# Optimization experiments

Hardware: AMD Instinct MI355X
Metric: run time of the kernel (lower is better)

## Reference

```python
import jax, jax.numpy as jnp
import numpy as np

B, L, H, K = 16, 2048, 1024, 4  # batch, seq, hidden, heads
NEG = -1e9  # stand-in for -inf in masked softmax (grad-safe, prob ~0)

def setup_inputs() -> dict:
    key = jax.random.key(0)
    ks = jax.random.split(key, 6)
    s = 0.02
    hidden = jax.random.normal(ks[0], (B, L, H), dtype=jnp.float32)
    masks = jax.random.randint(ks[1], (B, L), 0, 2).astype(jnp.bool_)
    Wp = jax.random.normal(ks[2], (H, H * K), dtype=jnp.float32) * s
    W1 = jax.random.normal(ks[3], (K, H, H // 2), dtype=jnp.float32) * s
    b1 = jax.random.normal(ks[4], (K, H // 2), dtype=jnp.float32) * s
    W2 = jax.random.normal(ks[5], (K, H // 2), dtype=jnp.float32) * s
    return {"hidden": hidden, "masks": masks, "Wp": Wp, "W1": W1, "b1": b1, "W2": W2}

def reference(hidden, masks, Wp, W1, b1, W2):
    b, l, h = hidden.shape
    k = W1.shape[0]
    # projection (no bias), split into heads: [b,l,k,h]
    proj = (hidden @ Wp).reshape(b, l, k, h)
    # per-head tanh MLP score: Linear(h, h//2)+bias -> tanh -> Linear(h//2, 1)
    a1 = jnp.tanh(jnp.einsum('blkh,khd->blkd', proj, W1) + b1)  # [b,l,k,h//2]
    logits = jnp.einsum('blkd,kd->kbl', a1, W2)                 # [k,b,l]
    # masked softmax over sequence dim
    logits = jnp.where(masks[None, :, :], NEG, logits)
    attn = jax.nn.softmax(logits, axis=-1)                      # [k,b,l]
    return attn
```

## Files before the change

### kernel.cpp

```cpp
#include <hip/hip_runtime.h>
#include <hip/hip_bf16.h>
#include <cstdint>
#include <cstddef>

#define HD   1024
#define NK   4
#define DD   512
#define LSEQ 2048
#define NB   16
#define MTOT (NB*LSEQ)
#define NF2  (NK*DD)

typedef __attribute__((ext_vector_type(4))) float f32x4;
typedef __attribute__((ext_vector_type(8))) short bf16x8;

#define GLOAD16(gp, lp) __builtin_amdgcn_global_load_lds( \
    (const __attribute__((address_space(1))) void*)(gp),  \
    (__attribute__((address_space(3))) void*)(lp), 16, 0, 0)

static __device__ __forceinline__ ushort f2bf(float f) {
  union { float f; unsigned u; } x; x.f = f;
  unsigned r = x.u + 0x7FFFu + ((x.u >> 16) & 1u);
  return (ushort)(r >> 16);
}

static __device__ __forceinline__ float fast_tanh(float x) {
  x = fminf(fmaxf(x, -15.f), 15.f);
  float t = __expf(2.0f * x);
  return (t - 1.0f) / (t + 1.0f);
}

__global__ void detect_mask_kernel(const unsigned char* __restrict__ m, int nbytes,
                                   int* __restrict__ flag) {
  int found = 0;
  for (int i = blockIdx.x * blockDim.x + threadIdx.x; i < nbytes;
       i += gridDim.x * blockDim.x)
    if ((i & 3) && m[i]) found = 1;
  if (__any(found) && (threadIdx.x & 63) == 0) atomicOr(flag, 1);
}

__global__ void cvt_f32_bf16_kernel(const float* __restrict__ src,
                                    ushort* __restrict__ dst, long n) {
  long stride = (long)gridDim.x * blockDim.x * 4;
  for (long i = ((long)blockIdx.x * blockDim.x + threadIdx.x) * 4; i < n; i += stride) {
    f32x4 v = *(const f32x4*)(src + i);
    ushort4 o; o.x = f2bf(v.x); o.y = f2bf(v.y); o.z = f2bf(v.z); o.w = f2bf(v.w);
    *(ushort4*)(dst + i) = o;
  }
}

__global__ void cvt_wp_heads_kernel(const float* __restrict__ Wp,
                                    ushort* __restrict__ WpH) {
  long i4 = ((long)blockIdx.x * blockDim.x + threadIdx.x) * 4;
  int h = (int)(i4 >> 20);
  int c = (int)((i4 >> 10) & 1023);
  int j = (int)(i4 & 1023);
  f32x4 v = *(const f32x4*)(Wp + (long)c * (NK * HD) + h * HD + j);
  ushort4 o; o.x = f2bf(v.x); o.y = f2bf(v.y); o.z = f2bf(v.z); o.w = f2bf(v.w);
  *(ushort4*)(WpH + i4) = o;
}

__global__ void transpose_cvt_kernel(const float* __restrict__ src,
                                     ushort* __restrict__ dst,
                                     int R, int C, long sBatch, long dBatch) {
  __shared__ float tile[32][33];
  const float* s = src + blockIdx.z * sBatch;
  ushort* d = dst + blockIdx.z * dBatch;
  int c0 = blockIdx.x * 32, r0 = blockIdx.y * 32;
  int tx = threadIdx.x, ty = threadIdx.y;
  #pragma unroll
  for (int i = 0; i < 32; i += 8)
    tile[ty + i][tx] = s[(long)(r0 + ty + i) * C + (c0 + tx)];
  __syncthreads();
  #pragma unroll
  for (int i = 0; i < 32; i += 8)
    d[(long)(c0 + ty + i) * R + (r0 + tx)] = f2bf(tile[tx][ty + i]);
}

template<int MODE>
__global__ __launch_bounds__(512, 2)
void gemm256_kernel(const ushort* __restrict__ A, int lda, long aZs,
                    const ushort* __restrict__ Bt, int ldb, long bZs, int Kdim,
                    ushort* __restrict__ Cout, int ldc, long cZs,
                    const float* __restrict__ b1, const float* __restrict__ W2,
                    float* __restrict__ logitsOut, int m0glob) {
  __shared__ __align__(16) char lds[131072];

  const int tid = threadIdx.x;
  const int w = tid >> 6, lane = tid & 63;
  const int z = blockIdx.z;

  int bid = blockIdx.x + gridDim.x * blockIdx.y;
  const int nwg = gridDim.x * gridDim.y;
  if ((nwg & 7) == 0) {
    const int q = nwg >> 3;
    bid = (bid & 7) * q + (bid >> 3);
  }
  const int nMB = gridDim.x;
  const int m0 = (bid % nMB) * 256;
  const int n0 = (bid / nMB) * 256;

  const ushort* Ag = A + z * aZs + (long)m0 * lda;
  const ushort* Bg = Bt + z * bZs + (long)n0 * ldb;

  const int wm = w >> 2, wn = w & 3;
  const int rsel = lane & 15;
  const int chunkC = ((lane >> 4) ^ ((rsel >> 1) & 3)) << 4;
  const int laneA = wm * 8192 + rsel * 64 + chunkC;
  const int laneB = 65536 + wn * 4096 + rsel * 64 + chunkC;

  const int stCg = ((lane & 3) ^ ((lane >> 3) & 3)) * 8;
  const int stR0 = (w * 2) * 16 + (lane >> 2);
  const int stDst0 = (w * 2) * 1024;

  #define STAGE(gbase, ld, regionByte, dsl, h)                                  \
    {                                                                           \
      _Pragma("unroll")                                                         \
      for (int j = 0; j < 2; ++j) {                                             \
        const ushort* gp = (gbase) + (long)(stR0 + j * 16) * (ld) +             \
                           ((h) << 5) + stCg;                                   \
        GLOAD16(gp, lds + (regionByte) + (dsl) * 16384 + stDst0 + j * 1024);    \
      }                                                                         \
    }

  f32x4 acc[8][4] = {};
  const int nph = Kdim >> 5;

  #pragma unroll
  for (int h = 0; h < 3; ++h) {
    STAGE(Ag, lda, 0,     h, h);
    STAGE(Bg, ldb, 65536, h, h);
  }
  asm volatile("s_waitcnt vmcnt(4)" ::: "memory");
  __builtin_amdgcn_sched_barrier(0);
  __builtin_amdgcn_s_barrier();

  bf16x8 aCur[8], bCur[4], aNxt[8], bNxt[4];
  #pragma unroll
  for (int nf = 0; nf < 4; ++nf) bCur[nf] = *(const bf16x8*)(lds + laneB + nf * 1024);
  #pragma unroll
  for (int f = 0; f < 8; ++f)    aCur[f] = *(const bf16x8*)(lds + laneA + f * 1024);

  #define PHASE(g, CA, CB, NA, NB_)                                             \
    {                                                                           \
      const int dsl = ((g) + 3) & 3;                                            \
      const int hh = ((g) + 3 < nph) ? (g) + 3 : nph - 1;                       \
      STAGE(Ag, lda, 0,     dsl, hh);                                           \
      STAGE(Bg, ldb, 65536, dsl, hh);                                           \
      const int rs = (((g) + 1) & 3) << 14;                                     \
      _Pragma("unroll")                                                         \
      for (int nf = 0; nf < 4; ++nf)                                            \
        NB_[nf] = *(const bf16x8*)(lds + rs + laneB + nf * 1024);               \
      _Pragma("unroll")                                                         \
      for (int f = 0; f < 8; ++f)                                               \
        NA[f] = *(const bf16x8*)(lds + rs + laneA + f * 1024);                  \
      asm volatile("s_waitcnt lgkmcnt(12)" ::: "memory");                       \
      __builtin_amdgcn_sched_barrier(0);                                        \
      __builtin_amdgcn_s_setprio(1);                                            \
      _Pragma("unroll")                                                         \
      for (int f = 0; f < 8; ++f)                                               \
        _Pragma("unroll")                                                       \
        for (int nf = 0; nf < 4; ++nf)                                          \
          acc[f][nf] = __builtin_amdgcn_mfma_f32_16x16x32_bf16(                 \
              CA[f], CB[nf], acc[f][nf], 0, 0, 0);                              \
      __builtin_amdgcn_s_setprio(0);                                            \
      asm volatile("s_waitcnt vmcnt(4)" ::: "memory");                          \
      __builtin_amdgcn_sched_barrier(0);                                        \
      __builtin_amdgcn_s_barrier();                                             \
    }

  for (int g = 0; g < nph; g += 2) {
    PHASE(g,     aCur, bCur, aNxt, bNxt);
    PHASE(g + 1, aNxt, bNxt, aCur, bCur);
  }
  asm volatile("s_waitcnt vmcnt(0)" ::: "memory");

  if constexpr (MODE == 0) {
    #pragma unroll
    for (int mf = 0; mf < 8; ++mf)
      #pragma unroll
      for (int nf = 0; nf < 4; ++nf) {
        const int col = n0 + wn * 64 + nf * 16 + (lane & 15);
        #pragma unroll
        for (int r = 0; r < 4; ++r) {
          const int row = m0 + wm * 128 + mf * 16 + ((lane >> 4) << 2) + r;
          Cout[z * cZs + (long)row * ldc + col] = f2bf(acc[mf][nf][r]);
        }
      }
  } else {
    float b1v[4], w2v[4];
    #pragma unroll
    for (int nf = 0; nf < 4; ++nf) {
      const int col = n0 + wn * 64 + nf * 16 + (lane & 15);
      b1v[nf] = b1[col];
      w2v[nf] = W2[col];
    }
    const long headBase = (long)((n0 + wn * 64) >> 9) * MTOT + m0glob;
    #pragma unroll
    for (int mf = 0; mf < 8; ++mf)
      #pragma unroll
      for (int r = 0; r < 4; ++r) {
        float s = 0.f;
        #pragma unroll
        for (int nf = 0; nf < 4; ++nf)
          s += fast_tanh(acc[mf][nf][r] + b1v[nf]) * w2v[nf];
        s += __shfl_xor(s, 1, 64);
        s += __shfl_xor(s, 2, 64);
        s += __shfl_xor(s, 4, 64);
        s += __shfl_xor(s, 8, 64);
        if ((lane & 15) == 0) {
          const int row = m0 + wm * 128 + mf * 16 + ((lane >> 4) << 2) + r;
          atomicAdd(&logitsOut[headBase + row], s);
        }
      }
  }
  #undef PHASE
  #undef STAGE
}

__global__ __launch_bounds__(256)
void masked_softmax_kernel(const float* __restrict__ logits,
                           const unsigned char* __restrict__ maskB,
                           const int* __restrict__ maskI,
                           const int* __restrict__ flag,
                           float* __restrict__ out) {
  const int kb = blockIdx.x;
  const int b = kb & (NB - 1);
  const long base = (long)kb * LSEQ;
  const bool isByte = (*flag != 0);
  const int tid = threadIdx.x;

  float x[8];
  float mx = -3.0e38f;
  #pragma unroll
  for (int j = 0; j < 8; ++j) {
    int l = tid + j * 256;
    bool msk = isByte ? (maskB[b * LSEQ + l] != 0) : (maskI[b * LSEQ + l] != 0);
    float v = msk ? -1e9f : logits[base + l];
    x[j] = v; mx = fmaxf(mx, v);
  }
  __shared__ float redm[4], reds[4];
  #pragma unroll
  for (int off = 32; off >= 1; off >>= 1) mx = fmaxf(mx, __shfl_xor(mx, off, 64));
  if ((tid & 63) == 0) redm[tid >> 6] = mx;
  __syncthreads();
  mx = fmaxf(fmaxf(redm[0], redm[1]), fmaxf(redm[2], redm[3]));

  float sum = 0.f;
  #pragma unroll
  for (int j = 0; j < 8; ++j) { x[j] = __expf(x[j] - mx); sum += x[j]; }
  #pragma unroll
  for (int off = 32; off >= 1; off >>= 1) sum += __shfl_xor(sum, off, 64);
  if ((tid & 63) == 0) reds[tid >> 6] = sum;
  __syncthreads();
  sum = reds[0] + reds[1] + reds[2] + reds[3];

  float inv = 1.0f / sum;
  #pragma unroll
  for (int j = 0; j < 8; ++j) out[base + tid + j * 256] = x[j] * inv;
}

extern "C" void kernel_launch(void* const* d_in, const int* in_sizes, int n_in,
                              void* d_out, int out_size, void* d_ws, size_t ws_size,
                              hipStream_t stream) {
  const float* hidden = (const float*)d_in[0];
  const void*  masks  = d_in[1];
  const float* Wp     = (const float*)d_in[2];
  const float* W1     = (const float*)d_in[3];
  const float* b1     = (const float*)d_in[4];
  const float* W2     = (const float*)d_in[5];
  float* out = (float*)d_out;

  char* ws = (char*)d_ws;
  ushort* W1T      = (ushort*)(ws + 0);
  ushort* WpH      = (ushort*)(ws + 4194304);
  ushort* WfT      = (ushort*)(ws + 12582912);
  float*  logits   = (float*) (ws + 16777216);
  int*    flag     = (int*)   (ws + 17301504);
  ushort* hiddenBf = (ushort*)(ws + 17301760);

  const size_t fixedBytes = 17301760;
  size_t avail = (ws_size > fixedBytes) ? (ws_size - fixedBytes) : 0;
  long chunkM = (long)(avail / ((long)HD * 2)) & ~255L;
  if (chunkM > MTOT) chunkM = MTOT;
  if (chunkM < 256) chunkM = 256;

  hipMemsetAsync(ws + 16777216, 0, 524288 + 256, stream);

  detect_mask_kernel<<<8, 256, 0, stream>>>((const unsigned char*)masks, NB * LSEQ, flag);

  dim3 tb(32, 8);
  transpose_cvt_kernel<<<dim3(DD / 32, HD / 32, NK), tb, 0, stream>>>(
      W1, W1T, HD, DD, (long)HD * DD, (long)DD * HD);
  cvt_wp_heads_kernel<<<4096, 256, 0, stream>>>(Wp, WpH);

  gemm256_kernel<0><<<dim3(2, 4, 4), 512, 0, stream>>>(
      W1T, HD, (long)DD * HD,
      WpH, HD, (long)HD * HD, HD,
      WfT, HD, (long)DD * HD,
      nullptr, nullptr, nullptr, 0);

  for (long m0 = 0; m0 < MTOT; m0 += chunkM) {
    long cm = chunkM; if (m0 + cm > MTOT) cm = MTOT - m0;
    cvt_f32_bf16_kernel<<<2048, 256, 0, stream>>>(
        hidden + m0 * HD, hiddenBf, cm * HD);
    gemm256_kernel<1><<<dim3(cm / 256, NF2 / 256, 1), 512, 0, stream>>>(
        hiddenBf, HD, 0,
        WfT, HD, 0, HD,
        nullptr, 0, 0,
        b1, W2, logits, (int)m0);
  }

  masked_softmax_kernel<<<NK * NB, 256, 0, stream>>>(
      logits, (const unsigned char*)masks, (const int*)masks, flag, out);
}
```

Baseline: 257.9 us.

## Restructure GEMM mainloop into 8-wave quadrant phases with K=64 double-buffered tiles

Replaces the 4-slot K=32 LDS ring with a double-buffered K=64 tile split into half-tiles. The main loop now runs eight phases per iteration, each computing one quadrant of the output. Each phase loads only the A/B fragments it needs and issues one half-tile global-to-LDS stage, interleaving loads with MFMA work in the style of an HipKittens 8-wave ping-pong. The LDS swizzle, the warp-to-output mapping and the epilogue indexing change to match. It adds more barriers per K-step and waits on lgkmcnt(0) before each MFMA group, trading the earlier register prefetch for finer interleaving.

```diff
diff --git a/kernel.cpp b/kernel.cpp
--- a/kernel.cpp
+++ b/kernel.cpp
@@ -103,119 +103,144 @@
   const ushort* Ag = A + z * aZs + (long)m0 * lda;
   const ushort* Bg = Bt + z * bZs + (long)n0 * ldb;
 
-  const int wm = w >> 2, wn = w & 3;
-  const int rsel = lane & 15;
-  const int chunkC = ((lane >> 4) ^ ((rsel >> 1) & 3)) << 4;
-  const int laneA = wm * 8192 + rsel * 64 + chunkC;
-  const int laneB = 65536 + wn * 4096 + rsel * 64 + chunkC;
-
-  const int stCg = ((lane & 3) ^ ((lane >> 3) & 3)) * 8;
-  const int stR0 = (w * 2) * 16 + (lane >> 2);
-  const int stDst0 = (w * 2) * 1024;
-
-  #define STAGE(gbase, ld, regionByte, dsl, h)                                  \
+  const int r = w >> 2, c = w & 3;
+  const int rsel = lane & 15, ch = lane >> 4;
+
+  const int sw0 = ((ch ^ (rsel & 7)) << 4);
+  const int baseA0 = r * 8192 + rsel * 128 + sw0;
+  const int baseA1 = baseA0 ^ 64;
+  const int baseB0 = 65536 + c * 4096 + rsel * 128 + sw0;
+  const int baseB1 = baseB0 ^ 64;
+
+  const int stRow = lane >> 3;
+  const int stCol = ((lane & 7) ^ (lane >> 3)) * 8;
+
+  #define STG(REG, GP, LD, SBUF, SHALF, SKT)                                    \
     {                                                                           \
       _Pragma("unroll")                                                         \
-      for (int j = 0; j < 2; ++j) {                                             \
-        const ushort* gp = (gbase) + (long)(stR0 + j * 16) * (ld) +             \
-                           ((h) << 5) + stCg;                                   \
-        GLOAD16(gp, lds + (regionByte) + (dsl) * 16384 + stDst0 + j * 1024);    \
+      for (int jj = 0; jj < 2; ++jj) {                                          \
+        const ushort* gsrc = (GP) +                                             \
+            (long)((SHALF) * 128 + w * 16 + jj * 8 + stRow) * (LD) +            \
+            (SKT) * 64 + stCol;                                                 \
+        GLOAD16(gsrc, lds + (REG) + (SBUF) * 32768 + (SHALF) * 16384 +          \
+                (w * 2 + jj) * 1024);                                           \
       }                                                                         \
     }
 
   f32x4 acc[8][4] = {};
-  const int nph = Kdim >> 5;
-
-  #pragma unroll
-  for (int h = 0; h < 3; ++h) {
-    STAGE(Ag, lda, 0,     h, h);
-    STAGE(Bg, ldb, 65536, h, h);
-  }
+  bf16x8 aF[4][2], bB[2][2][2];
+
+  #define PHASE(BUF, MH, NH, LA, LB, SREG, SGP, SLD, SBUF, SHALF, SKT, VM)      \
+    {                                                                           \
+      if (LA) {                                                                 \
+        _Pragma("unroll")                                                       \
+        for (int mf = 0; mf < 4; ++mf) {                                        \
+          aF[mf][0] = *(const bf16x8*)(lds + (BUF) * 32768 + (MH) * 16384 +     \
+                                       mf * 2048 + baseA0);                     \
+          aF[mf][1] = *(const bf16x8*)(lds + (BUF) * 32768 + (MH) * 16384 +     \
+                                       mf * 2048 + baseA1);                     \
+        }                                                                       \
+      }                                                                         \
+      if (LB) {                                                                 \
+        _Pragma("unroll")                                                       \
+        for (int nf = 0; nf < 2; ++nf) {                                        \
+          bB[NH][nf][0] = *(const bf16x8*)(lds + (BUF) * 32768 + (NH) * 16384 + \
+                                           nf * 2048 + baseB0);                 \
+          bB[NH][nf][1] = *(const bf16x8*)(lds + (BUF) * 32768 + (NH) * 16384 + \
+                                           nf * 2048 + baseB1);                 \
+        }                                                                       \
+      }                                                                         \
+      STG(SREG, SGP, SLD, SBUF, SHALF, SKT);                                    \
+      __builtin_amdgcn_s_barrier();                                             \
+      asm volatile("s_waitcnt lgkmcnt(0)" ::: "memory");                        \
+      __builtin_amdgcn_sched_barrier(0);                                        \
+      __builtin_amdgcn_s_setprio(1);                                            \
+      _Pragma("unroll")                                                         \
+      for (int ks = 0; ks < 2; ++ks)                                            \
+        _Pragma("unroll")                                                       \
+        for (int mf = 0; mf < 4; ++mf)                                          \
+          _Pragma("unroll")                                                     \
+          for (int nf = 0; nf < 2; ++nf)                                        \
+            acc[(MH)*4+mf][(NH)*2+nf] =                                         \
+                __builtin_amdgcn_mfma_f32_16x16x32_bf16(                        \
+                    aF[mf][ks], bB[NH][nf][ks], acc[(MH)*4+mf][(NH)*2+nf],      \
+                    0, 0, 0);                                                   \
+      __builtin_amdgcn_s_setprio(0);                                            \
+      if (VM) {                                                                 \
+        asm volatile("s_waitcnt vmcnt(4)" ::: "memory");                        \
+        __builtin_amdgcn_sched_barrier(0);                                      \
+      }                                                                         \
+      __builtin_amdgcn_s_barrier();                                             \
+    }
+
+  const int ntk = Kdim >> 6;
+  const int nt2 = Kdim >> 7;
+
+  STG(0,     Ag, lda, 0, 0, 0);
+  STG(65536, Bg, ldb, 0, 0, 0);
+  STG(65536, Bg, ldb, 0, 1, 0);
+  STG(0,     Ag, lda, 0, 1, 0);
   asm volatile("s_waitcnt vmcnt(4)" ::: "memory");
   __builtin_amdgcn_sched_barrier(0);
   __builtin_amdgcn_s_barrier();
 
-  bf16x8 aCur[8], bCur[4], aNxt[8], bNxt[4];
-  #pragma unroll
-  for (int nf = 0; nf < 4; ++nf) bCur[nf] = *(const bf16x8*)(lds + laneB + nf * 1024);
-  #pragma unroll
-  for (int f = 0; f < 8; ++f)    aCur[f] = *(const bf16x8*)(lds + laneA + f * 1024);
-
-  #define PHASE(g, CA, CB, NA, NB_)                                             \
-    {                                                                           \
-      const int dsl = ((g) + 3) & 3;                                            \
-      const int hh = ((g) + 3 < nph) ? (g) + 3 : nph - 1;                       \
-      STAGE(Ag, lda, 0,     dsl, hh);                                           \
-      STAGE(Bg, ldb, 65536, dsl, hh);                                           \
-      const int rs = (((g) + 1) & 3) << 14;                                     \
-      _Pragma("unroll")                                                         \
-      for (int nf = 0; nf < 4; ++nf)                                            \
-        NB_[nf] = *(const bf16x8*)(lds + rs + laneB + nf * 1024);               \
-      _Pragma("unroll")                                                         \
-      for (int f = 0; f < 8; ++f)                                               \
-        NA[f] = *(const bf16x8*)(lds + rs + laneA + f * 1024);                  \
-      asm volatile("s_waitcnt lgkmcnt(12)" ::: "memory");                       \
-      __builtin_amdgcn_sched_barrier(0);                                        \
-      __builtin_amdgcn_s_setprio(1);                                            \
-      _Pragma("unroll")                                                         \
-      for (int f = 0; f < 8; ++f)                                               \
-        _Pragma("unroll")                                                       \
-        for (int nf = 0; nf < 4; ++nf)                                          \
-          acc[f][nf] = __builtin_amdgcn_mfma_f32_16x16x32_bf16(                 \
-              CA[f], CB[nf], acc[f][nf], 0, 0, 0);                              \
-      __builtin_amdgcn_s_setprio(0);                                            \
-      asm volatile("s_waitcnt vmcnt(4)" ::: "memory");                          \
-      __builtin_amdgcn_sched_barrier(0);                                        \
-      __builtin_amdgcn_s_barrier();                                             \
-    }
-
-  for (int g = 0; g < nph; g += 2) {
-    PHASE(g,     aCur, bCur, aNxt, bNxt);
-    PHASE(g + 1, aNxt, bNxt, aCur, bCur);
+  for (int j = 0; j < nt2; ++j) {
+    const int k1 = 2 * j + 1;
+    const int k2 = (2 * j + 2 < ntk) ? (2 * j + 2) : (ntk - 1);
+    PHASE(0, 0, 0, 1, 1, 0,     Ag, lda, 1, 0, k1, 1)
+    PHASE(0, 0, 1, 0, 1, 65536, Bg, ldb, 1, 0, k1, 1)
+    PHASE(0, 1, 1, 1, 0, 65536, Bg, ldb, 1, 1, k1, 0)
+    PHASE(0, 1, 0, 0, 0, 0,     Ag, lda, 1, 1, k1, 1)
+    PHASE(1, 0, 0, 1, 1, 0,     Ag, lda, 0, 0, k2, 1)
+    PHASE(1, 0, 1, 0, 1, 65536, Bg, ldb, 0, 0, k2, 1)
+    PHASE(1, 1, 1, 1, 0, 65536, Bg, ldb, 0, 1, k2, 0)
+    PHASE(1, 1, 0, 0, 0, 0,     Ag, lda, 0, 1, k2, 1)
   }
   asm volatile("s_waitcnt vmcnt(0)" ::: "memory");
 
   if constexpr (MODE == 0) {
     #pragma unroll
-    for (int mf = 0; mf < 8; ++mf)
+    for (int am = 0; am < 8; ++am)
       #pragma unroll
-      for (int nf = 0; nf < 4; ++nf) {
-        const int col = n0 + wn * 64 + nf * 16 + (lane & 15);
+      for (int an = 0; an < 4; ++an) {
+        const int col = n0 + (an >> 1) * 128 + c * 32 + (an & 1) * 16 + (lane & 15);
         #pragma unroll
-        for (int r = 0; r < 4; ++r) {
-          const int row = m0 + wm * 128 + mf * 16 + ((lane >> 4) << 2) + r;
-          Cout[z * cZs + (long)row * ldc + col] = f2bf(acc[mf][nf][r]);
+        for (int rr = 0; rr < 4; ++rr) {
+          const int row = m0 + (am >> 2) * 128 + r * 64 + (am & 3) * 16 +
+                          ((lane >> 4) << 2) + rr;
+          Cout[z * cZs + (long)row * ldc + col] = f2bf(acc[am][an][rr]);
         }
       }
   } else {
     float b1v[4], w2v[4];
     #pragma unroll
-    for (int nf = 0; nf < 4; ++nf) {
-      const int col = n0 + wn * 64 + nf * 16 + (lane & 15);
-      b1v[nf] = b1[col];
-      w2v[nf] = W2[col];
+    for (int an = 0; an < 4; ++an) {
+      const int col = n0 + (an >> 1) * 128 + c * 32 + (an & 1) * 16 + (lane & 15);
+      b1v[an] = b1[col];
+      w2v[an] = W2[col];
     }
-    const long headBase = (long)((n0 + wn * 64) >> 9) * MTOT + m0glob;
+    const long headBase = (long)(n0 >> 9) * MTOT + m0glob + m0;
     #pragma unroll
-    for (int mf = 0; mf < 8; ++mf)
+    for (int am = 0; am < 8; ++am)
       #pragma unroll
-      for (int r = 0; r < 4; ++r) {
+      for (int rr = 0; rr < 4; ++rr) {
         float s = 0.f;
         #pragma unroll
-        for (int nf = 0; nf < 4; ++nf)
-          s += fast_tanh(acc[mf][nf][r] + b1v[nf]) * w2v[nf];
+        for (int an = 0; an < 4; ++an)
+          s += fast_tanh(acc[am][an][rr] + b1v[an]) * w2v[an];
         s += __shfl_xor(s, 1, 64);
         s += __shfl_xor(s, 2, 64);
         s += __shfl_xor(s, 4, 64);
         s += __shfl_xor(s, 8, 64);
         if ((lane & 15) == 0) {
-          const int row = m0 + wm * 128 + mf * 16 + ((lane >> 4) << 2) + r;
+          const int row = (am >> 2) * 128 + r * 64 + (am & 3) * 16 +
+                          ((lane >> 4) << 2) + rr;
           atomicAdd(&logitsOut[headBase + row], s);
         }
       }
   }
   #undef PHASE
-  #undef STAGE
+  #undef STG
 }
 
 __global__ __launch_bounds__(256)
```

After: 246.8 us. 1.04x faster.

## Restructure GEMM main loop into 64-wide K tiles with quarter-phase interleaved staging

Applied to the files above, without the earlier changes.

Replaces the 3-deep prefetch of 32-wide K slices, with its double-buffered register fragments, by a loop over 64-wide K tiles. Each tile is split into four quarter phases that load half the A fragments, issue one global-to-LDS stage, and run 16 MFMAs. The change is meant to cut register pressure from holding two full fragment sets and to spread global loads evenly among the compute phases. In exchange it adds more barriers per K step, lowers the prefetch depth to two slices, and drops the overlap of LDS reads with MFMAs. The epilogue row indexing is also refactored so m0 is folded into the base offset.

```diff
diff --git a/kernel.cpp b/kernel.cpp
--- a/kernel.cpp
+++ b/kernel.cpp
@@ -113,65 +113,63 @@
   const int stR0 = (w * 2) * 16 + (lane >> 2);
   const int stDst0 = (w * 2) * 1024;
 
-  #define STAGE(gbase, ld, regionByte, dsl, h)                                  \
+  #define STAGE(gbase, ld, regionByte, dsl, ktile, kh)                          \
     {                                                                           \
       _Pragma("unroll")                                                         \
       for (int j = 0; j < 2; ++j) {                                             \
         const ushort* gp = (gbase) + (long)(stR0 + j * 16) * (ld) +             \
-                           ((h) << 5) + stCg;                                   \
+                           ((ktile) << 6) + ((kh) << 5) + stCg;                 \
         GLOAD16(gp, lds + (regionByte) + (dsl) * 16384 + stDst0 + j * 1024);    \
       }                                                                         \
     }
 
   f32x4 acc[8][4] = {};
-  const int nph = Kdim >> 5;
-
-  #pragma unroll
-  for (int h = 0; h < 3; ++h) {
-    STAGE(Ag, lda, 0,     h, h);
-    STAGE(Bg, ldb, 65536, h, h);
-  }
+
+  STAGE(Ag, lda, 0,     0, 0, 0);
+  STAGE(Bg, ldb, 65536, 0, 0, 0);
+  STAGE(Ag, lda, 0,     1, 0, 1);
+  STAGE(Bg, ldb, 65536, 1, 0, 1);
   asm volatile("s_waitcnt vmcnt(4)" ::: "memory");
   __builtin_amdgcn_sched_barrier(0);
   __builtin_amdgcn_s_barrier();
 
-  bf16x8 aCur[8], bCur[4], aNxt[8], bNxt[4];
-  #pragma unroll
-  for (int nf = 0; nf < 4; ++nf) bCur[nf] = *(const bf16x8*)(lds + laneB + nf * 1024);
-  #pragma unroll
-  for (int f = 0; f < 8; ++f)    aCur[f] = *(const bf16x8*)(lds + laneA + f * 1024);
-
-  #define PHASE(g, CA, CB, NA, NB_)                                             \
-    {                                                                           \
-      const int dsl = ((g) + 3) & 3;                                            \
-      const int hh = ((g) + 3 < nph) ? (g) + 3 : nph - 1;                       \
-      STAGE(Ag, lda, 0,     dsl, hh);                                           \
-      STAGE(Bg, ldb, 65536, dsl, hh);                                           \
-      const int rs = (((g) + 1) & 3) << 14;                                     \
-      _Pragma("unroll")                                                         \
-      for (int nf = 0; nf < 4; ++nf)                                            \
-        NB_[nf] = *(const bf16x8*)(lds + rs + laneB + nf * 1024);               \
-      _Pragma("unroll")                                                         \
-      for (int f = 0; f < 8; ++f)                                               \
-        NA[f] = *(const bf16x8*)(lds + rs + laneA + f * 1024);                  \
-      asm volatile("s_waitcnt lgkmcnt(12)" ::: "memory");                       \
-      __builtin_amdgcn_sched_barrier(0);                                        \
-      __builtin_amdgcn_s_setprio(1);                                            \
-      _Pragma("unroll")                                                         \
-      for (int f = 0; f < 8; ++f)                                               \
-        _Pragma("unroll")                                                       \
-        for (int nf = 0; nf < 4; ++nf)                                          \
-          acc[f][nf] = __builtin_amdgcn_mfma_f32_16x16x32_bf16(                 \
-              CA[f], CB[nf], acc[f][nf], 0, 0, 0);                              \
-      __builtin_amdgcn_s_setprio(0);                                            \
-      asm volatile("s_waitcnt vmcnt(4)" ::: "memory");                          \
-      __builtin_amdgcn_sched_barrier(0);                                        \
-      __builtin_amdgcn_s_barrier();                                             \
+  const int nt = Kdim >> 6;
+  for (int t = 0; t < nt; ++t) {
+    const int ts = (t + 1 < nt) ? t + 1 : t;
+    const int s0 = (2 * t) & 3, s1 = (2 * t + 1) & 3;
+    const int p0 = (2 * t + 2) & 3, p1 = (2 * t + 3) & 3;
+    bf16x8 aF[4], bB[4];
+    #pragma unroll
+    for (int q = 0; q < 4; ++q) {
+      const int kk = q >> 1, mh = q & 1;
+      const int slot = (kk ? s1 : s0) * 16384;
+      if (mh == 0) {
+        #pragma unroll
+        for (int nf = 0; nf < 4; ++nf)
+          bB[nf] = *(const bf16x8*)(lds + slot + laneB + nf * 1024);
+      }
+      #pragma unroll
+      for (int mf = 0; mf < 4; ++mf)
+        aF[mf] = *(const bf16x8*)(lds + slot + laneA + mh * 4096 + mf * 1024);
+      if (q == 0)      STAGE(Ag, lda, 0,     p0, ts, 0)
+      else if (q == 1) STAGE(Bg, ldb, 65536, p0, ts, 0)
+      else if (q == 2) STAGE(Ag, lda, 0,     p1, ts, 1)
+      else             STAGE(Bg, ldb, 65536, p1, ts, 1)
+      __builtin_amdgcn_s_barrier();
+      __builtin_amdgcn_s_setprio(1);
+      #pragma unroll
+      for (int mf = 0; mf < 4; ++mf)
+        #pragma unroll
+        for (int nf = 0; nf < 4; ++nf)
+          acc[mh * 4 + mf][nf] = __builtin_amdgcn_mfma_f32_16x16x32_bf16(
+              aF[mf], bB[nf], acc[mh * 4 + mf][nf], 0, 0, 0);
+      __builtin_amdgcn_s_setprio(0);
+      if (q & 1) {
+        asm volatile("s_waitcnt vmcnt(4)" ::: "memory");
+        __builtin_amdgcn_sched_barrier(0);
+      }
+      __builtin_amdgcn_s_barrier();
     }
-
-  for (int g = 0; g < nph; g += 2) {
-    PHASE(g,     aCur, bCur, aNxt, bNxt);
-    PHASE(g + 1, aNxt, bNxt, aCur, bCur);
   }
   asm volatile("s_waitcnt vmcnt(0)" ::: "memory");
 
@@ -195,7 +193,7 @@
       b1v[nf] = b1[col];
       w2v[nf] = W2[col];
     }
-    const long headBase = (long)((n0 + wn * 64) >> 9) * MTOT + m0glob;
+    const long headBase = (long)((n0 + wn * 64) >> 9) * MTOT + m0glob + m0;
     #pragma unroll
     for (int mf = 0; mf < 8; ++mf)
       #pragma unroll
@@ -209,12 +207,11 @@
         s += __shfl_xor(s, 4, 64);
         s += __shfl_xor(s, 8, 64);
         if ((lane & 15) == 0) {
-          const int row = m0 + wm * 128 + mf * 16 + ((lane >> 4) << 2) + r;
+          const int row = wm * 128 + mf * 16 + ((lane >> 4) << 2) + r;
           atomicAdd(&logitsOut[headBase + row], s);
         }
       }
   }
-  #undef PHASE
   #undef STAGE
 }
 
```

Result: no change. 257.6 us (-0.1%).
